# Kernel optimization log

Measured on AMD Instinct MI355X. Metric: run time of the kernel, lower is better.

## Reference

```python
import jax, jax.numpy as jnp
import numpy as np

N = 50000      # nodes in the block
M = 10         # mailbox_size
H = 8          # attention heads
DIN = 128      # dim_in (per-mail message dim)
DOUT = 128     # dim_out (memory dim)
DT = 128       # dim_time
LN_EPS = 1e-5
LRELU_SLOPE = 0.2


def setup_inputs() -> dict:
    key = jax.random.key(0)
    ks = jax.random.split(key, 16)
    s = 0.05  # small init scale for weights
    return {
        # forward tensor args
        "mem": jax.random.normal(ks[0], (N, DOUT), jnp.float32),
        "mem_input": jax.random.normal(ks[1], (N, M * DIN), jnp.float32),
        "ts": jax.random.uniform(ks[2], (N,), jnp.float32) * 100.0,
        "mail_ts": jax.random.uniform(ks[3], (N, M), jnp.float32) * 100.0,
        # learned parameters (torch Linear convention: W is [out, in])
        "wq_w": jax.random.normal(ks[4], (DOUT, DOUT), jnp.float32) * s,
        "wq_b": jnp.zeros((DOUT,), jnp.float32),
        "wk_w": jax.random.normal(ks[5], (DOUT, DIN + DT), jnp.float32) * s,
        "wk_b": jnp.zeros((DOUT,), jnp.float32),
        "wv_w": jax.random.normal(ks[6], (DOUT, DIN + DT), jnp.float32) * s,
        "wv_b": jnp.zeros((DOUT,), jnp.float32),
        "ln_g": jnp.ones((DOUT,), jnp.float32),
        "ln_b": jnp.zeros((DOUT,), jnp.float32),
        "mlp_w": jax.random.normal(ks[7], (DOUT, DOUT), jnp.float32) * s,
        "mlp_b": jnp.zeros((DOUT,), jnp.float32),
        # TimeEncode: cos(dt * te_w + te_b), te_w = 1/10^linspace(0,9,DT) as in TGN
        "te_w": (1.0 / (10.0 ** np.linspace(0, 9, DT))).astype(np.float32),
        "te_b": jnp.zeros((DT,), jnp.float32),
    }


def reference(mem, mem_input, ts, mail_ts,
              wq_w, wq_b, wk_w, wk_b, wv_w, wv_b,
              ln_g, ln_b, mlp_w, mlp_b, te_w, te_b):
    n = mem.shape[0]
    # Q: [n, H, Dh]
    Q = (mem @ wq_w.T + wq_b).reshape(n, H, -1)
    # mails: [n, M, DIN]
    mails = mem_input.reshape(n, M, -1)
    # time encoding of (src ts - mail ts): [n, M, DT]
    dt = ts[:, None] - mail_ts
    time_feat = jnp.cos(dt[:, :, None] * te_w + te_b)
    mails = jnp.concatenate([mails, time_feat], axis=2)  # [n, M, DIN+DT]
    K = (mails @ wk_w.T + wk_b).reshape(n, M, H, -1)
    V = (mails @ wv_w.T + wv_b).reshape(n, M, H, -1)
    # elementwise QK reduction over head dim, LeakyReLU, softmax over mailbox
    att = jnp.einsum('nhd,nmhd->nmh', Q, K)
    att = jax.nn.leaky_relu(att, LRELU_SLOPE)
    att = jax.nn.softmax(att, axis=1)          # (att_dropout = identity in eval)
    rst = jnp.einsum('nmh,nmhd->nhd', att, V).reshape(n, -1)
    rst = rst + mem                             # residual
    # LayerNorm
    mu = rst.mean(axis=-1, keepdims=True)
    var = ((rst - mu) ** 2).mean(axis=-1, keepdims=True)
    rst = (rst - mu) / jnp.sqrt(var + LN_EPS) * ln_g + ln_b
    # MLP + (dropout = identity in eval) + ReLU
    rst = rst @ mlp_w.T + mlp_b
    return jax.nn.relu(rst)
```

## Files before the change

kernel.cpp:

```cpp
#include <hip/hip_runtime.h>
#include <hip/hip_bf16.h>

#define N_NODES 50000
#define NB 32
#define LN_EPS 1e-5f
#define SLOPE 0.2f

typedef __attribute__((ext_vector_type(8))) short bf16x8;
typedef __attribute__((ext_vector_type(4))) float f32x4;

__device__ __forceinline__ int imin(int a, int b){ return a < b ? a : b; }

__device__ __forceinline__ short f2bf(float f){
  union { float f; unsigned u; } v; v.f = f;
  unsigned r = v.u + 0x7fffu + ((v.u >> 16) & 1u);
  return (short)(r >> 16);
}

__device__ __forceinline__ float rsum16_dpp(float x){
  asm volatile(
    "s_nop 1\n\t"
    "v_add_f32_dpp %0, %0, %0 row_ror:8 row_mask:0xf bank_mask:0xf\n\t"
    "s_nop 1\n\t"
    "v_add_f32_dpp %0, %0, %0 row_ror:4 row_mask:0xf bank_mask:0xf\n\t"
    "s_nop 1\n\t"
    "v_add_f32_dpp %0, %0, %0 row_ror:2 row_mask:0xf bank_mask:0xf\n\t"
    "s_nop 1\n\t"
    "v_add_f32_dpp %0, %0, %0 row_ror:1 row_mask:0xf bank_mask:0xf"
    : "+v"(x));
  return x;
}

__device__ __forceinline__ unsigned cvtpk(float a, float b){
  unsigned r;
  asm("v_cvt_pk_bf16_f32 %0, %1, %2" : "=v"(r) : "v"(a), "v"(b));
  return r;
}

__device__ __forceinline__ bf16x8 pack8(float4 a, float4 b){
  union { unsigned u[4]; bf16x8 v; } r;
  r.u[0] = cvtpk(a.x, a.y); r.u[1] = cvtpk(a.z, a.w);
  r.u[2] = cvtpk(b.x, b.y); r.u[3] = cvtpk(b.z, b.w);
  return r.v;
}

#define WKP 0
#define WVP 32768
#define WQP 65536
#define MLPP 81920

__global__ __launch_bounds__(256) void prep_pack(
    const float* __restrict__ wq, const float* __restrict__ wk,
    const float* __restrict__ wv, const float* __restrict__ mlp,
    unsigned short* __restrict__ wsP)
{
  int idx = blockIdx.x * 256 + threadIdx.x;
  const float* src; int base, K, local;
  if (idx < 32768)      { src = wk;  base = WKP;  local = idx;         K = 256; }
  else if (idx < 65536) { src = wv;  base = WVP;  local = idx - 32768; K = 256; }
  else if (idx < 81920) { src = wq;  base = WQP;  local = idx - 65536; K = 128; }
  else if (idx < 98304) { src = mlp; base = MLPP; local = idx - 81920; K = 128; }
  else return;
  int i  = local & 7;
  int l  = (local >> 3) & 63;
  int nt = (local >> 9) & 7;
  int ks = local >> 12;
  int row = nt * 16 + (l & 15);
  int k   = ks * 32 + ((l >> 4) << 3) + i;
  wsP[base + local] = (unsigned short)f2bf(src[row * K + k]);
}

__device__ __forceinline__ void stage_write(
    unsigned short* sAp, const float* sTs, const float* sMts,
    const float* sTeW, const float* sTeB,
    float4 f0, float4 f1, int srow, int skc, int ssw, int sg, int m)
{
  float dt = sTs[srow] - sMts[srow*10 + m];
  const float4* tw = (const float4*)(sTeW + skc);
  const float4* tb = (const float4*)(sTeB + skc);
  float4 w0 = tw[0], w1 = tw[1];
  float4 b0 = tb[0], b1 = tb[1];
  float4 c0, c1;
  c0.x=__cosf(dt*w0.x+b0.x); c0.y=__cosf(dt*w0.y+b0.y); c0.z=__cosf(dt*w0.z+b0.z); c0.w=__cosf(dt*w0.w+b0.w);
  c1.x=__cosf(dt*w1.x+b1.x); c1.y=__cosf(dt*w1.y+b1.y); c1.z=__cosf(dt*w1.z+b1.z); c1.w=__cosf(dt*w1.w+b1.w);
  bf16x8* dst = (bf16x8*)sAp;
  dst[srow*32 + (sg ^ ssw)]      = pack8(f0, f1);
  dst[srow*32 + 16 + (sg ^ ssw)] = pack8(c0, c1);
}

__global__ __launch_bounds__(512, 2) void fused_tmu(
    const float* __restrict__ mem, const float* __restrict__ mem_input,
    const float* __restrict__ ts, const float* __restrict__ mail_ts,
    const float* __restrict__ wq_b, const float* __restrict__ wk_b,
    const float* __restrict__ wv_b, const float* __restrict__ ln_g,
    const float* __restrict__ ln_b, const float* __restrict__ mlp_b,
    const float* __restrict__ te_w, const float* __restrict__ te_b,
    const unsigned short* __restrict__ wsP, float* __restrict__ out)
{
  __shared__ __align__(16) unsigned short sA[2 * NB * 256];
  __shared__ float sTs[NB];
  __shared__ float sMts[NB * 10];
  __shared__ float sTeW[128], sTeB[128];
  __shared__ float sRed[NB * 16];

  const int tid  = threadIdx.x;
  const int lane = tid & 63;
  const int wid  = tid >> 6;
  const int l15  = lane & 15;
  const int lg   = lane >> 4;
  const int node0 = blockIdx.x * NB;

  const int srow = tid >> 4;
  const int sg   = tid & 15;
  const int skc  = sg << 3;
  const int sgn  = imin(node0 + srow, N_NODES - 1);
  const int ssw  = srow & 7;
  const float* miBase = mem_input + (size_t)sgn * 1280 + skc;

  float4 fm0, fm1, fa0, fa1;
  {
    const float4* mp = (const float4*)(mem + (size_t)sgn * 128 + skc);
    fm0 = mp[0]; fm1 = mp[1];
    const float4* mi0 = (const float4*)(miBase);
    fa0 = mi0[0]; fa1 = mi0[1];
  }

  if (tid < NB) sTs[tid] = ts[imin(node0 + tid, N_NODES - 1)];
  if (tid < 128){ sTeW[tid] = te_w[tid]; sTeB[tid] = te_b[tid]; }
  if (tid < NB * 10){
    int nn = tid / 10, mm = tid - nn * 10;
    sMts[tid] = mail_ts[(size_t)imin(node0 + nn, N_NODES - 1) * 10 + mm];
  }
  {
    bf16x8* dst = (bf16x8*)sA;
    dst[NB*32 + srow*32 + (sg ^ ssw)] = pack8(fm0, fm1);
  }

  const int c = wid * 16 + l15;
  float qb = wq_b[c], kb = wk_b[c], vb = wv_b[c];

  const bf16x8* wsv = (const bf16x8*)wsP;
  bf16x8 wqf[4];
  #pragma unroll
  for (int ks = 0; ks < 4; ks++)
    wqf[ks] = wsv[WQP/8 + (ks*8 + wid)*64 + lane];

  __syncthreads();

  stage_write(sA, sTs, sMts, sTeW, sTeB, fa0, fa1, srow, skc, ssw, sg, 0);
  { const float4* mi1 = (const float4*)(miBase + 128); fa0 = mi1[0]; fa1 = mi1[1]; }

  f32x4 z4 = {0.f, 0.f, 0.f, 0.f};
  f32x4 qac[2];
  qac[0] = (f32x4){qb, qb, qb, qb};
  qac[1] = qac[0];
  {
    const bf16x8* P1 = (const bf16x8*)sA + NB*32;
    #pragma unroll
    for (int ntr = 0; ntr < 2; ntr++){
      int r = ntr*16 + l15, rs = r & 7;
      #pragma unroll
      for (int ks = 0; ks < 4; ks++){
        bf16x8 af = P1[r*32 + ((ks*4 + lg) ^ rs)];
        qac[ntr] = __builtin_amdgcn_mfma_f32_16x16x32_bf16(af, wqf[ks], qac[ntr], 0, 0, 0);
      }
    }
  }

  bf16x8 wkf[8], wvf[8];
  #pragma unroll
  for (int ks = 0; ks < 8; ks++){
    wkf[ks] = wsv[WKP/8 + (ks*8 + wid)*64 + lane];
    wvf[ks] = wsv[WVP/8 + (ks*8 + wid)*64 + lane];
  }

  __syncthreads();

  f32x4 pv[2] = {z4, z4};
  f32x4 sm[2] = {z4, z4};
  for (int m = 0; m < 10; m++){
    const bf16x8* P = (const bf16x8*)sA + (m & 1) * NB*32;
    #pragma unroll
    for (int ntr = 0; ntr < 2; ntr++){
      int r = ntr*16 + l15, rs = r & 7;
      f32x4 ka = z4, va = z4;
      #pragma unroll
      for (int ks = 0; ks < 8; ks++){
        bf16x8 af = P[r*32 + ((ks*4 + lg) ^ rs)];
        ka = __builtin_amdgcn_mfma_f32_16x16x32_bf16(af, wkf[ks], ka, 0, 0, 0);
        va = __builtin_amdgcn_mfma_f32_16x16x32_bf16(af, wvf[ks], va, 0, 0, 0);
      }
      #pragma unroll
      for (int j = 0; j < 4; j++){
        float lv = (ka[j] + kb) * qac[ntr][j];
        lv = rsum16_dpp(lv);
        lv = fmaxf(lv, SLOPE * lv);
        lv = fminf(lv, 60.f);
        float p = __expf(lv);
        sm[ntr][j] += p;
        pv[ntr][j] += p * va[j];
      }
    }
    if (m < 9){
      stage_write(sA + ((m+1) & 1) * NB*256, sTs, sMts, sTeW, sTeB,
                  fa0, fa1, srow, skc, ssw, sg, m+1);
      if (m < 8){
        const float4* mi = (const float4*)(miBase + (size_t)(m+2)*128);
        fa0 = mi[0]; fa1 = mi[1];
      }
    }
    __syncthreads();
  }

  float lgv = ln_g[c], lbv = ln_b[c], mbv = mlp_b[c];
  float rstv[2][4];
  #pragma unroll
  for (int ntr = 0; ntr < 2; ntr++)
    #pragma unroll
    for (int j = 0; j < 4; j++){
      int gn = imin(node0 + ntr*16 + lg*4 + j, N_NODES - 1);
      rstv[ntr][j] = pv[ntr][j] / sm[ntr][j] + vb + mem[(size_t)gn * 128 + c];
    }
  #pragma unroll
  for (int ntr = 0; ntr < 2; ntr++)
    #pragma unroll
    for (int j = 0; j < 4; j++){
      float s = rsum16_dpp(rstv[ntr][j]);
      float q = rsum16_dpp(rstv[ntr][j] * rstv[ntr][j]);
      if (l15 == 0){
        int nl = ntr*16 + lg*4 + j;
        sRed[nl*16 + wid*2    ] = s;
        sRed[nl*16 + wid*2 + 1] = q;
      }
    }
  __syncthreads();
  #pragma unroll
  for (int ntr = 0; ntr < 2; ntr++)
    #pragma unroll
    for (int j = 0; j < 4; j++){
      int nl = ntr*16 + lg*4 + j;
      float sum = 0.f, sq = 0.f;
      #pragma unroll
      for (int w = 0; w < 8; w++){
        sum += sRed[nl*16 + w*2];
        sq  += sRed[nl*16 + w*2 + 1];
      }
      float mu  = sum * (1.f/128.f);
      float var = sq * (1.f/128.f) - mu*mu;
      float rs  = rsqrtf(var + LN_EPS);
      float y = (rstv[ntr][j] - mu) * rs * lgv + lbv;
      sA[nl*256 + ((c >> 3) ^ (nl & 7))*8 + (c & 7)] = (unsigned short)f2bf(y);
    }

  bf16x8 mlpf[4];
  #pragma unroll
  for (int ks = 0; ks < 4; ks++)
    mlpf[ks] = wsv[MLPP/8 + (ks*8 + wid)*64 + lane];
  __syncthreads();

  f32x4 mac[2];
  mac[0] = (f32x4){mbv, mbv, mbv, mbv};
  mac[1] = mac[0];
  {
    const bf16x8* P0 = (const bf16x8*)sA;
    #pragma unroll
    for (int ntr = 0; ntr < 2; ntr++){
      int r = ntr*16 + l15, rs = r & 7;
      #pragma unroll
      for (int ks = 0; ks < 4; ks++){
        bf16x8 af = P0[r*32 + ((ks*4 + lg) ^ rs)];
        mac[ntr] = __builtin_amdgcn_mfma_f32_16x16x32_bf16(af, mlpf[ks], mac[ntr], 0, 0, 0);
      }
    }
  }
  #pragma unroll
  for (int ntr = 0; ntr < 2; ntr++)
    #pragma unroll
    for (int j = 0; j < 4; j++){
      float o = fmaxf(mac[ntr][j], 0.f);
      int node = node0 + ntr*16 + lg*4 + j;
      if (node < N_NODES)
        out[(size_t)node * 128 + c] = o;
    }
}

extern "C" void kernel_launch(void* const* d_in, const int* in_sizes, int n_in,
                              void* d_out, int out_size, void* d_ws, size_t ws_size,
                              hipStream_t stream)
{
  const float* mem       = (const float*)d_in[0];
  const float* mem_input = (const float*)d_in[1];
  const float* ts        = (const float*)d_in[2];
  const float* mail_ts   = (const float*)d_in[3];
  const float* wq_w      = (const float*)d_in[4];
  const float* wq_b      = (const float*)d_in[5];
  const float* wk_w      = (const float*)d_in[6];
  const float* wk_b      = (const float*)d_in[7];
  const float* wv_w      = (const float*)d_in[8];
  const float* wv_b      = (const float*)d_in[9];
  const float* ln_g      = (const float*)d_in[10];
  const float* ln_b      = (const float*)d_in[11];
  const float* mlp_w     = (const float*)d_in[12];
  const float* mlp_b     = (const float*)d_in[13];
  const float* te_w      = (const float*)d_in[14];
  const float* te_b      = (const float*)d_in[15];
  unsigned short* wsP = (unsigned short*)d_ws;
  float* outp = (float*)d_out;

  prep_pack<<<384, 256, 0, stream>>>(wq_w, wk_w, wv_w, mlp_w, wsP);
  int nblk = (N_NODES + NB - 1) / NB;
  fused_tmu<<<nblk, 512, 0, stream>>>(mem, mem_input, ts, mail_ts,
      wq_b, wk_b, wv_b, ln_g, ln_b, mlp_b, te_w, te_b, wsP, outp);
}
```

Baseline: 146.3 us.

## Process two mailbox slots per iteration with a four-buffer LDS ring

The mailbox loop now handles two mail slots per iteration, using a four-stage shared-memory ring in place of double buffering. The next pair of slots is staged before the current pair is computed, and two sets of K/V MFMA chains are interleaved. This halves the number of block-wide barriers and gives the scheduler more independent MFMA and DPP work to overlap. In exchange, LDS use for the staging buffer doubles and register pressure rises from the extra prefetch registers and accumulators, which could cause spills under the 512-thread, 2-block launch bounds.

```diff
diff --git a/kernel.cpp b/kernel.cpp
--- a/kernel.cpp
+++ b/kernel.cpp
@@ -97,7 +97,7 @@
     const float* __restrict__ te_w, const float* __restrict__ te_b,
     const unsigned short* __restrict__ wsP, float* __restrict__ out)
 {
-  __shared__ __align__(16) unsigned short sA[2 * NB * 256];
+  __shared__ __align__(16) unsigned short sA[4 * NB * 256];
   __shared__ float sTs[NB];
   __shared__ float sMts[NB * 10];
   __shared__ float sTeW[128], sTeB[128];
@@ -117,12 +117,14 @@
   const int ssw  = srow & 7;
   const float* miBase = mem_input + (size_t)sgn * 1280 + skc;
 
-  float4 fm0, fm1, fa0, fa1;
+  float4 fm0, fm1, fa0, fa1, fb0, fb1;
   {
     const float4* mp = (const float4*)(mem + (size_t)sgn * 128 + skc);
     fm0 = mp[0]; fm1 = mp[1];
     const float4* mi0 = (const float4*)(miBase);
     fa0 = mi0[0]; fa1 = mi0[1];
+    const float4* mi1 = (const float4*)(miBase + 128);
+    fb0 = mi1[0]; fb1 = mi1[1];
   }
 
   if (tid < NB) sTs[tid] = ts[imin(node0 + tid, N_NODES - 1)];
@@ -133,7 +135,7 @@
   }
   {
     bf16x8* dst = (bf16x8*)sA;
-    dst[NB*32 + srow*32 + (sg ^ ssw)] = pack8(fm0, fm1);
+    dst[2*NB*32 + srow*32 + (sg ^ ssw)] = pack8(fm0, fm1);
   }
 
   const int c = wid * 16 + l15;
@@ -147,21 +149,27 @@
 
   __syncthreads();
 
-  stage_write(sA, sTs, sMts, sTeW, sTeB, fa0, fa1, srow, skc, ssw, sg, 0);
-  { const float4* mi1 = (const float4*)(miBase + 128); fa0 = mi1[0]; fa1 = mi1[1]; }
+  stage_write(sA,            sTs, sMts, sTeW, sTeB, fa0, fa1, srow, skc, ssw, sg, 0);
+  stage_write(sA + NB*256,   sTs, sMts, sTeW, sTeB, fb0, fb1, srow, skc, ssw, sg, 1);
+  {
+    const float4* mi2 = (const float4*)(miBase + 2*128);
+    fa0 = mi2[0]; fa1 = mi2[1];
+    const float4* mi3 = (const float4*)(miBase + 3*128);
+    fb0 = mi3[0]; fb1 = mi3[1];
+  }
 
   f32x4 z4 = {0.f, 0.f, 0.f, 0.f};
   f32x4 qac[2];
   qac[0] = (f32x4){qb, qb, qb, qb};
   qac[1] = qac[0];
   {
-    const bf16x8* P1 = (const bf16x8*)sA + NB*32;
+    const bf16x8* P2 = (const bf16x8*)sA + 2*NB*32;
     #pragma unroll
     for (int ntr = 0; ntr < 2; ntr++){
       int r = ntr*16 + l15, rs = r & 7;
       #pragma unroll
       for (int ks = 0; ks < 4; ks++){
-        bf16x8 af = P1[r*32 + ((ks*4 + lg) ^ rs)];
+        bf16x8 af = P2[r*32 + ((ks*4 + lg) ^ rs)];
         qac[ntr] = __builtin_amdgcn_mfma_f32_16x16x32_bf16(af, wqf[ks], qac[ntr], 0, 0, 0);
       }
     }
@@ -178,35 +186,47 @@
 
   f32x4 pv[2] = {z4, z4};
   f32x4 sm[2] = {z4, z4};
-  for (int m = 0; m < 10; m++){
-    const bf16x8* P = (const bf16x8*)sA + (m & 1) * NB*32;
+  for (int t = 0; t < 5; t++){
+    if (t < 4){
+      stage_write(sA + ((2*t+2) & 3) * NB*256, sTs, sMts, sTeW, sTeB,
+                  fa0, fa1, srow, skc, ssw, sg, 2*t+2);
+      stage_write(sA + ((2*t+3) & 3) * NB*256, sTs, sMts, sTeW, sTeB,
+                  fb0, fb1, srow, skc, ssw, sg, 2*t+3);
+      if (t < 3){
+        const float4* miA = (const float4*)(miBase + (size_t)(2*t+4)*128);
+        fa0 = miA[0]; fa1 = miA[1];
+        const float4* miB = (const float4*)(miBase + (size_t)(2*t+5)*128);
+        fb0 = miB[0]; fb1 = miB[1];
+      }
+    }
+    const bf16x8* Pa = (const bf16x8*)sA + ((2*t) & 3) * NB*32;
+    const bf16x8* Pb = (const bf16x8*)sA + ((2*t+1) & 3) * NB*32;
     #pragma unroll
     for (int ntr = 0; ntr < 2; ntr++){
       int r = ntr*16 + l15, rs = r & 7;
-      f32x4 ka = z4, va = z4;
+      f32x4 ka0 = z4, va0 = z4, ka1 = z4, va1 = z4;
       #pragma unroll
       for (int ks = 0; ks < 8; ks++){
-        bf16x8 af = P[r*32 + ((ks*4 + lg) ^ rs)];
-        ka = __builtin_amdgcn_mfma_f32_16x16x32_bf16(af, wkf[ks], ka, 0, 0, 0);
-        va = __builtin_amdgcn_mfma_f32_16x16x32_bf16(af, wvf[ks], va, 0, 0, 0);
+        int idx = r*32 + ((ks*4 + lg) ^ rs);
+        bf16x8 af0 = Pa[idx];
+        bf16x8 af1 = Pb[idx];
+        ka0 = __builtin_amdgcn_mfma_f32_16x16x32_bf16(af0, wkf[ks], ka0, 0, 0, 0);
+        ka1 = __builtin_amdgcn_mfma_f32_16x16x32_bf16(af1, wkf[ks], ka1, 0, 0, 0);
+        va0 = __builtin_amdgcn_mfma_f32_16x16x32_bf16(af0, wvf[ks], va0, 0, 0, 0);
+        va1 = __builtin_amdgcn_mfma_f32_16x16x32_bf16(af1, wvf[ks], va1, 0, 0, 0);
       }
       #pragma unroll
       for (int j = 0; j < 4; j++){
-        float lv = (ka[j] + kb) * qac[ntr][j];
-        lv = rsum16_dpp(lv);
-        lv = fmaxf(lv, SLOPE * lv);
-        lv = fminf(lv, 60.f);
-        float p = __expf(lv);
-        sm[ntr][j] += p;
-        pv[ntr][j] += p * va[j];
-      }
-    }
-    if (m < 9){
-      stage_write(sA + ((m+1) & 1) * NB*256, sTs, sMts, sTeW, sTeB,
-                  fa0, fa1, srow, skc, ssw, sg, m+1);
-      if (m < 8){
-        const float4* mi = (const float4*)(miBase + (size_t)(m+2)*128);
-        fa0 = mi[0]; fa1 = mi[1];
+        float lv0 = (ka0[j] + kb) * qac[ntr][j];
+        float lv1 = (ka1[j] + kb) * qac[ntr][j];
+        lv0 = rsum16_dpp(lv0);
+        lv1 = rsum16_dpp(lv1);
+        lv0 = fmaxf(lv0, SLOPE * lv0); lv0 = fminf(lv0, 60.f);
+        lv1 = fmaxf(lv1, SLOPE * lv1); lv1 = fminf(lv1, 60.f);
+        float p0 = __expf(lv0);
+        float p1 = __expf(lv1);
+        sm[ntr][j] += p0 + p1;
+        pv[ntr][j] += p0 * va0[j] + p1 * va1[j];
       }
     }
     __syncthreads();
```

Result: no change. 148.9 us (+1.8%).
